# Optimization experiments

Hardware: AMD Instinct MI355X
Metric: run time of the kernel (lower is better)

Reference implementation:

```python
import jax, jax.numpy as jnp
import numpy as np

B, N, C, H = 16, 4096, 256, 4
D = C // H


def setup_inputs() -> dict:
    key = jax.random.key(0)
    ks = jax.random.split(key, 16)
    s = 0.02
    inp = {
        "x": jax.random.normal(ks[0], (B, N, C), jnp.float32),
        "encoding": jax.random.normal(ks[1], (2, B, 1, N, D), jnp.float32),
        "Wqkv_w": jax.random.normal(ks[2], (3 * C, C), jnp.float32) * s,
        "Wqkv_b": jnp.zeros((3 * C,), jnp.float32),
        "tssa_qkv_w": jax.random.normal(ks[3], (C, C), jnp.float32) * s,
        "tssa_qkv_b": jnp.zeros((C,), jnp.float32),
        "temp": jnp.ones((H, 1), jnp.float32),
        "tssa_out_w": jax.random.normal(ks[4], (C, C), jnp.float32) * s,
        "tssa_out_b": jnp.zeros((C,), jnp.float32),
        "out_proj_w": jax.random.normal(ks[5], (C, C), jnp.float32) * s,
        "out_proj_b": jnp.zeros((C,), jnp.float32),
        "ffn1_w": jax.random.normal(ks[6], (2 * C, 2 * C), jnp.float32) * s,
        "ffn1_b": jnp.zeros((2 * C,), jnp.float32),
        "ln_g": jnp.ones((2 * C,), jnp.float32),
        "ln_b": jnp.zeros((2 * C,), jnp.float32),
        "ffn2_w": jax.random.normal(ks[7], (C, 2 * C), jnp.float32) * s,
        "ffn2_b": jnp.zeros((C,), jnp.float32),
    }
    return inp


def _rotate_half(t):
    # (..., d) -> pairwise rotate: (x1, x2) -> (-x2, x1)
    t2 = t.reshape(t.shape[:-1] + (-1, 2))
    x1, x2 = t2[..., 0], t2[..., 1]
    return jnp.stack((-x2, x1), axis=-1).reshape(t.shape)


def reference(x, encoding, Wqkv_w, Wqkv_b, tssa_qkv_w, tssa_qkv_b, temp,
              tssa_out_w, tssa_out_b, out_proj_w, out_proj_b,
              ffn1_w, ffn1_b, ln_g, ln_b, ffn2_w, ffn2_b):
    b, n, c = x.shape
    h, d = H, D
    # QKV projection, layout (h, d, 3) on last dim as in unflatten(-1,(h,-1,3))
    qkv = (x @ Wqkv_w.T + Wqkv_b).reshape(b, n, h, d, 3).transpose(0, 2, 1, 3, 4)  # b h n d 3
    q, k, v = qkv[..., 0], qkv[..., 1], qkv[..., 2]
    rope = lambda t: t * encoding[0] + _rotate_half(t) * encoding[1]
    q = rope(q)
    k = rope(k)
    flat = lambda t: t.transpose(0, 2, 1, 3).reshape(b, n, c)  # b h n d -> b n (h d)
    w_input = (flat(q) + flat(k) + flat(v)) / 3.0
    # TSSA attention
    w = (w_input @ tssa_qkv_w.T + tssa_qkv_b).reshape(b, n, h, d).transpose(0, 2, 1, 3)  # b h n d
    norm = jnp.sqrt(jnp.sum(w * w, axis=2, keepdims=True))  # L2 over sequence axis N
    w_normed = w / jnp.maximum(norm, 1e-12)
    sum_ws = jnp.sum(w_normed * w_normed, axis=-1)  # b h n
    Pi = jax.nn.softmax(sum_ws * temp[None, :, :], axis=1)  # softmax over heads
    Pi_norm = Pi / (jnp.sum(Pi, axis=-1, keepdims=True) + 1e-8)
    dots = jnp.einsum('bhn,bhnd->bh', Pi_norm, w * w)  # (b,h,1,d) summed over d
    attn = 1.0 / (1.0 + dots)  # b h
    out = -(w * Pi[..., None]) * attn[:, :, None, None]  # b h n d
    out = out.transpose(0, 2, 1, 3).reshape(b, n, c)
    context = out @ tssa_out_w.T + tssa_out_b
    message = context @ out_proj_w.T + out_proj_b
    # residual FFN
    cat = jnp.concatenate([x, message], axis=-1)  # b n 2c
    h1 = cat @ ffn1_w.T + ffn1_b
    mu = jnp.mean(h1, axis=-1, keepdims=True)
    var = jnp.mean((h1 - mu) ** 2, axis=-1, keepdims=True)
    ln = (h1 - mu) / jnp.sqrt(var + 1e-5) * ln_g + ln_b
    g = jax.nn.gelu(ln, approximate=False)
    return x + (g @ ffn2_w.T + ffn2_b)
```

## Files before the change

### kernel.cpp

```cpp
#include <hip/hip_runtime.h>
#include <math.h>

#define Bc 16
#define Nc 4096

typedef __attribute__((ext_vector_type(8))) short short8;
typedef __attribute__((ext_vector_type(4))) float floatx4;

__device__ __forceinline__ unsigned short f2bf(float f) {
    union { float f; unsigned int u; } v; v.f = f;
    unsigned int u = v.u;
    return (unsigned short)((u + 0x7fffu + ((u >> 16) & 1u)) >> 16);
}
__device__ __forceinline__ float bf2f(unsigned short u) {
    union { unsigned int u; float f; } v; v.u = ((unsigned int)u) << 16;
    return v.f;
}

__device__ __forceinline__ void gll16(const unsigned short* g, unsigned short* l) {
    __builtin_amdgcn_global_load_lds(
        (const __attribute__((address_space(1))) void*)g,
        (__attribute__((address_space(3))) void*)l,
        16, 0, 0);
}

template <int EPI, typename TOUT>
__global__ __launch_bounds__(512) void gemm_bf(
    const unsigned short* __restrict__ A0, int lda0,
    const unsigned short* __restrict__ A1, int lda1, int K0,
    const unsigned short* __restrict__ W,
    const float* __restrict__ bias,
    const unsigned short* __restrict__ resid_bf,
    const float* __restrict__ Pi,
    const float* __restrict__ attnb,
    float* __restrict__ norm2,
    float* __restrict__ rowstats,
    TOUT* __restrict__ C, int N, int K)
{
    __shared__ alignas(16) unsigned short As[128 * 64];
    __shared__ alignas(16) unsigned short Bs[256 * 64];

    const int t = threadIdx.x;
    const int bn = blockIdx.x, bm = blockIdx.y;
    const int lane = t & 63, wave = t >> 6;
    const int wm = wave >> 2, wn = wave & 3;
    const int quad = lane >> 4, l16 = lane & 15;
    const int rt = t >> 3, st = t & 7;

    floatx4 acc[4][4];
    #pragma unroll
    for (int i = 0; i < 4; ++i)
        #pragma unroll
        for (int j = 0; j < 4; ++j)
            acc[i][j] = (floatx4){0.f, 0.f, 0.f, 0.f};

    for (int k0 = 0; k0 < K; k0 += 64) {
        #pragma unroll
        for (int hh = 0; hh < 2; ++hh) {
            const int row = hh * 64 + rt;
            const int col = k0 + (st ^ (row & 7)) * 8;
            unsigned short* ldsa = As + row * 64 + st * 8;
            const size_t grow = (size_t)bm * 128 + row;
            if constexpr (EPI == 2) {
                const int b = (int)(grow >> 12);
                const int hd = col >> 6;
                const float sc = -Pi[grow * 4 + hd] * attnb[b * 4 + hd];
                const short8 a = *(const short8*)(A0 + grow * (size_t)lda0 + col);
                short8 o;
                #pragma unroll
                for (int j = 0; j < 8; ++j) o[j] = (short)f2bf(bf2f((unsigned short)a[j]) * sc);
                *(short8*)ldsa = o;
            } else {
                const unsigned short* src = (col < K0)
                    ? (A0 + grow * (size_t)lda0 + col)
                    : (A1 + grow * (size_t)lda1 + (col - K0));
                gll16(src, ldsa);
            }
        }
        #pragma unroll
        for (int hh = 0; hh < 4; ++hh) {
            const int row = hh * 64 + rt;
            const int col = k0 + (st ^ (row & 7)) * 8;
            gll16(W + ((size_t)bn * 256 + row) * (size_t)K + col, Bs + row * 64 + st * 8);
        }
        __syncthreads();
        #pragma unroll
        for (int kk = 0; kk < 2; ++kk) {
            short8 af[4], wf[4];
            #pragma unroll
            for (int i = 0; i < 4; ++i) {
                const int ra = wm * 64 + i * 16 + l16;
                af[i] = *(const short8*)(As + ra * 64 + ((quad + kk * 4) ^ (ra & 7)) * 8);
                const int rw = wn * 64 + i * 16 + l16;
                wf[i] = *(const short8*)(Bs + rw * 64 + ((quad + kk * 4) ^ (rw & 7)) * 8);
            }
            #pragma unroll
            for (int mi = 0; mi < 4; ++mi)
                #pragma unroll
                for (int ni = 0; ni < 4; ++ni)
                    acc[mi][ni] = __builtin_amdgcn_mfma_f32_16x16x32_bf16(
                        wf[ni], af[mi], acc[mi][ni], 0, 0, 0);
        }
        __syncthreads();
    }

    float rs[4], rq[4];
    if constexpr (EPI == 4) {
        #pragma unroll
        for (int m = 0; m < 4; ++m) { rs[m] = 0.f; rq[m] = 0.f; }
    }

    #pragma unroll
    for (int mi = 0; mi < 4; ++mi) {
        const size_t row = (size_t)bm * 128 + wm * 64 + mi * 16 + l16;
        #pragma unroll
        for (int ni = 0; ni < 4; ++ni) {
            const int cb = bn * 256 + wn * 64 + ni * 16 + quad * 4;
            const float4 b4 = *(const float4*)(bias + cb);
            float v[4] = {acc[mi][ni][0] + b4.x, acc[mi][ni][1] + b4.y,
                          acc[mi][ni][2] + b4.z, acc[mi][ni][3] + b4.w};
            if constexpr (EPI == 3) {
                const ushort4 xr = *(const ushort4*)(resid_bf + row * (size_t)N + cb);
                v[0] += bf2f(xr.x); v[1] += bf2f(xr.y);
                v[2] += bf2f(xr.z); v[3] += bf2f(xr.w);
            }
            if constexpr (EPI == 4) {
                #pragma unroll
                for (int rg = 0; rg < 4; ++rg) { rs[mi] += v[rg]; rq[mi] += v[rg] * v[rg]; }
            }
            if constexpr (EPI == 1) {
                float cs[4];
                #pragma unroll
                for (int rg = 0; rg < 4; ++rg) cs[rg] = v[rg] * v[rg];
                #pragma unroll
                for (int rg = 0; rg < 4; ++rg) {
                    float s = cs[rg];
                    s += __shfl_xor(s, 1, 64);
                    s += __shfl_xor(s, 2, 64);
                    s += __shfl_xor(s, 4, 64);
                    s += __shfl_xor(s, 8, 64);
                    if (l16 == 0) atomicAdd(&norm2[(bm >> 5) * 256 + cb + rg], s);
                }
            }
            if constexpr (__is_same(TOUT, float)) {
                float4 o; o.x = v[0]; o.y = v[1]; o.z = v[2]; o.w = v[3];
                *(float4*)(C + row * (size_t)N + cb) = o;
            } else {
                ushort4 o;
                o.x = f2bf(v[0]); o.y = f2bf(v[1]); o.z = f2bf(v[2]); o.w = f2bf(v[3]);
                *(ushort4*)(C + row * (size_t)N + cb) = o;
            }
        }
    }
    if constexpr (EPI == 4) {
        #pragma unroll
        for (int mi = 0; mi < 4; ++mi) {
            float s = rs[mi], q = rq[mi];
            s += __shfl_xor(s, 16, 64); s += __shfl_xor(s, 32, 64);
            q += __shfl_xor(q, 16, 64); q += __shfl_xor(q, 32, 64);
            if (quad == 0) {
                const size_t row = (size_t)bm * 128 + wm * 64 + mi * 16 + l16;
                atomicAdd(&rowstats[row * 2], s);
                atomicAdd(&rowstats[row * 2 + 1], q);
            }
        }
    }
}

__global__ __launch_bounds__(256) void gemm_rope(
    const unsigned short* __restrict__ A,
    const unsigned short* __restrict__ Wsv,
    const float* __restrict__ bsv,
    const float* __restrict__ enc,
    unsigned short* __restrict__ wi)
{
    __shared__ alignas(16) unsigned short As[128 * 64];
    __shared__ alignas(16) unsigned short Ss[128 * 64];
    __shared__ alignas(16) unsigned short Vs[128 * 64];

    const int t = threadIdx.x;
    const int bn = blockIdx.x, bm = blockIdx.y;
    const int lane = t & 63, wave = t >> 6;
    const int wm = wave >> 1, wn = wave & 1;
    const int quad = lane >> 4, l16 = lane & 15;
    const int rt = t >> 3, st = t & 7;

    floatx4 accs[4][4], accv[4][4];
    #pragma unroll
    for (int i = 0; i < 4; ++i)
        #pragma unroll
        for (int j = 0; j < 4; ++j) {
            accs[i][j] = (floatx4){0.f, 0.f, 0.f, 0.f};
            accv[i][j] = (floatx4){0.f, 0.f, 0.f, 0.f};
        }

    for (int k0 = 0; k0 < 256; k0 += 64) {
        #pragma unroll
        for (int hh = 0; hh < 4; ++hh) {
            const int row = hh * 32 + rt;
            const int col = k0 + (st ^ (row & 7)) * 8;
            gll16(A + ((size_t)bm * 128 + row) * 256 + col, As + row * 64 + st * 8);
            gll16(Wsv + (size_t)(bn * 128 + row) * 256 + col, Ss + row * 64 + st * 8);
            gll16(Wsv + (size_t)(256 + bn * 128 + row) * 256 + col, Vs + row * 64 + st * 8);
        }
        __syncthreads();
        #pragma unroll
        for (int kk = 0; kk < 2; ++kk) {
            short8 af[4], sf[4], vf[4];
            #pragma unroll
            for (int i = 0; i < 4; ++i) {
                const int ra = wm * 64 + i * 16 + l16;
                af[i] = *(const short8*)(As + ra * 64 + ((quad + kk * 4) ^ (ra & 7)) * 8);
                const int rw = wn * 64 + i * 16 + l16;
                sf[i] = *(const short8*)(Ss + rw * 64 + ((quad + kk * 4) ^ (rw & 7)) * 8);
                vf[i] = *(const short8*)(Vs + rw * 64 + ((quad + kk * 4) ^ (rw & 7)) * 8);
            }
            #pragma unroll
            for (int mi = 0; mi < 4; ++mi)
                #pragma unroll
                for (int ni = 0; ni < 4; ++ni) {
                    accs[mi][ni] = __builtin_amdgcn_mfma_f32_16x16x32_bf16(sf[ni], af[mi], accs[mi][ni], 0, 0, 0);
                    accv[mi][ni] = __builtin_amdgcn_mfma_f32_16x16x32_bf16(vf[ni], af[mi], accv[mi][ni], 0, 0, 0);
                }
        }
        __syncthreads();
    }

    #pragma unroll
    for (int mi = 0; mi < 4; ++mi) {
        const size_t row = (size_t)bm * 128 + wm * 64 + mi * 16 + l16;
        #pragma unroll
        for (int ni = 0; ni < 4; ++ni) {
            const int cb = bn * 128 + wn * 64 + ni * 16 + quad * 4;
            const int d = cb & 63;
            const float s0 = accs[mi][ni][0] + bsv[cb];
            const float s1 = accs[mi][ni][1] + bsv[cb + 1];
            const float s2 = accs[mi][ni][2] + bsv[cb + 2];
            const float s3 = accs[mi][ni][3] + bsv[cb + 3];
            const float v0 = accv[mi][ni][0] + bsv[256 + cb];
            const float v1 = accv[mi][ni][1] + bsv[256 + cb + 1];
            const float v2 = accv[mi][ni][2] + bsv[256 + cb + 2];
            const float v3 = accv[mi][ni][3] + bsv[256 + cb + 3];
            const float4 e0q = *(const float4*)(enc + row * 64 + d);
            const float4 e1q = *(const float4*)(enc + 4194304 + row * 64 + d);
            const float r0 = s0 * e0q.x - s1 * e1q.x;
            const float r1 = s1 * e0q.y + s0 * e1q.y;
            const float r2 = s2 * e0q.z - s3 * e1q.z;
            const float r3 = s3 * e0q.w + s2 * e1q.w;
            ushort4 o;
            o.x = f2bf((r0 + v0) * (1.f / 3.f));
            o.y = f2bf((r1 + v1) * (1.f / 3.f));
            o.z = f2bf((r2 + v2) * (1.f / 3.f));
            o.w = f2bf((r3 + v3) * (1.f / 3.f));
            *(ushort4*)(wi + row * 256 + cb) = o;
        }
    }
}

__global__ __launch_bounds__(256) void lngelu_kernel(unsigned short* __restrict__ h1,
                                                     const float* __restrict__ rowstats,
                                                     const float* __restrict__ g,
                                                     const float* __restrict__ bb) {
    const size_t gid = (size_t)blockIdx.x * 256 + threadIdx.x;
    const size_t row = gid >> 6;
    const int col = (int)(gid & 63) * 8;
    const float2 stv = *(const float2*)(rowstats + row * 2);
    const float mean = stv.x * (1.f / 512.f);
    const float var = stv.y * (1.f / 512.f) - mean * mean;
    const float rstd = rsqrtf(var + 1e-5f);
    unsigned short* p = h1 + row * 512 + col;
    const short8 hv = *(const short8*)p;
    const float4 g0 = *(const float4*)(g + col);
    const float4 g1 = *(const float4*)(g + col + 4);
    const float4 b0 = *(const float4*)(bb + col);
    const float4 b1 = *(const float4*)(bb + col + 4);
    const float vg[8] = {g0.x, g0.y, g0.z, g0.w, g1.x, g1.y, g1.z, g1.w};
    const float vb[8] = {b0.x, b0.y, b0.z, b0.w, b1.x, b1.y, b1.z, b1.w};
    short8 ov;
    #pragma unroll
    for (int k = 0; k < 8; ++k) {
        const float ln = (bf2f((unsigned short)hv[k]) - mean) * rstd * vg[k] + vb[k];
        ov[k] = (short)f2bf(0.5f * ln * (1.f + erff(ln * 0.70710678118654752f)));
    }
    *(short8*)p = ov;
}

__device__ __forceinline__ void conv8(const float* src, unsigned short* dst, int i) {
    const float4 f0 = *(const float4*)(src + (size_t)i * 8);
    const float4 f1 = *(const float4*)(src + (size_t)i * 8 + 4);
    short8 sv;
    sv[0] = (short)f2bf(f0.x); sv[1] = (short)f2bf(f0.y);
    sv[2] = (short)f2bf(f0.z); sv[3] = (short)f2bf(f0.w);
    sv[4] = (short)f2bf(f1.x); sv[5] = (short)f2bf(f1.y);
    sv[6] = (short)f2bf(f1.z); sv[7] = (short)f2bf(f1.w);
    *(short8*)(dst + (size_t)i * 8) = sv;
}

__global__ __launch_bounds__(256) void prep_all(
    const float* __restrict__ x, const float* __restrict__ Wqkv,
    const float* __restrict__ bqkv, const float* __restrict__ tssa_w,
    const float* __restrict__ op_w, const float* __restrict__ to_w,
    const float* __restrict__ to_b, const float* __restrict__ op_b,
    const float* __restrict__ f1w, const float* __restrict__ f2w,
    unsigned short* __restrict__ x_bf, unsigned short* __restrict__ Wsv,
    float* __restrict__ bsv, unsigned short* __restrict__ tssa_bf,
    unsigned short* __restrict__ Wf, float* __restrict__ bfb,
    unsigned short* __restrict__ ffn1_bf, unsigned short* __restrict__ ffn2_bf,
    float* __restrict__ zbase, float* __restrict__ rowstats)
{
    const int blk = blockIdx.x, tt = threadIdx.x;
    if (blk < 8192) {
        conv8(x, x_bf, blk * 256 + tt);
    } else if (blk < 8704) {
        const int r = blk - 8192, c = tt;
        const int cd = r & 255;
        const int h = cd >> 6, dd = cd & 63;
        const int base = h * 192 + dd * 3;
        if (r < 256) {
            Wsv[r * 256 + c] = f2bf(Wqkv[(base + 0) * 256 + c] + Wqkv[(base + 1) * 256 + c]);
            if (c == 0) bsv[r] = bqkv[base] + bqkv[base + 1];
        } else {
            Wsv[r * 256 + c] = f2bf(Wqkv[(base + 2) * 256 + c]);
            if (c == 0) bsv[r] = bqkv[base + 2];
        }
    } else if (blk < 8960) {
        const int i = blk - 8704;
        float s = 0.f;
        for (int k = 0; k < 256; ++k) s += op_w[i * 256 + k] * to_w[k * 256 + tt];
        Wf[i * 256 + tt] = f2bf(s);
    } else if (blk == 8960) {
        float s = op_b[tt];
        for (int k = 0; k < 256; ++k) s += op_w[tt * 256 + k] * to_b[k];
        bfb[tt] = s;
    } else if (blk < 8993) {
        conv8(tssa_w, tssa_bf, (blk - 8961) * 256 + tt);
    } else if (blk < 9121) {
        conv8(f1w, ffn1_bf, (blk - 8993) * 256 + tt);
    } else if (blk < 9185) {
        conv8(f2w, ffn2_bf, (blk - 9121) * 256 + tt);
    } else {
        const int i = (blk - 9185) * 256 + tt;
        if (i < 4288) zbase[i] = 0.f;
        else if (i < 135360) rowstats[i - 4288] = 0.f;
    }
}

__global__ __launch_bounds__(256) void pi_kernel(const unsigned short* __restrict__ w,
                                                 const float* __restrict__ norm2,
                                                 const float* __restrict__ temp,
                                                 float* __restrict__ Pi,
                                                 float* __restrict__ S,
                                                 float* __restrict__ T) {
    const int t = threadIdx.x;
    const int i = t & 15;
    const int lr = t >> 4;
    const size_t r = (size_t)blockIdx.x * 16 + lr;
    const int b = (int)(r >> 12);
    const unsigned short* wrow = w + r * 256;
    const float* n2row = norm2 + b * 256;
    float raw[4], nrm[4];
    #pragma unroll
    for (int h = 0; h < 4; ++h) {
        const ushort4 wv = *(const ushort4*)(wrow + h * 64 + i * 4);
        const float w0 = bf2f(wv.x), w1 = bf2f(wv.y), w2 = bf2f(wv.z), w3 = bf2f(wv.w);
        const float4 n2 = *(const float4*)(n2row + h * 64 + i * 4);
        const float s0 = w0 * w0, s1 = w1 * w1, s2 = w2 * w2, s3 = w3 * w3;
        raw[h] = s0 + s1 + s2 + s3;
        nrm[h] = s0 / fmaxf(n2.x, 1e-24f) + s1 / fmaxf(n2.y, 1e-24f)
               + s2 / fmaxf(n2.z, 1e-24f) + s3 / fmaxf(n2.w, 1e-24f);
    }
    #pragma unroll
    for (int off = 1; off < 16; off <<= 1) {
        #pragma unroll
        for (int h = 0; h < 4; ++h) {
            raw[h] += __shfl_xor(raw[h], off, 64);
            nrm[h] += __shfl_xor(nrm[h], off, 64);
        }
    }
    float sw[4], m = -1e30f;
    #pragma unroll
    for (int h = 0; h < 4; ++h) { sw[h] = nrm[h] * temp[h]; m = fmaxf(m, sw[h]); }
    float e[4], Z = 0.f;
    #pragma unroll
    for (int h = 0; h < 4; ++h) { e[h] = expf(sw[h] - m); Z += e[h]; }
    const float invZ = 1.f / Z;
    float pi[4];
    #pragma unroll
    for (int h = 0; h < 4; ++h) pi[h] = e[h] * invZ;
    if (i < 4) Pi[r * 4 + i] = pi[i];

    __shared__ float sS[16][4], sT[16][4];
    if (i == 0) {
        #pragma unroll
        for (int h = 0; h < 4; ++h) { sS[lr][h] = pi[h]; sT[lr][h] = pi[h] * raw[h]; }
    }
    __syncthreads();
    if (t < 4) {
        float as = 0.f, at = 0.f;
        for (int rr = 0; rr < 16; ++rr) { as += sS[rr][t]; at += sT[rr][t]; }
        atomicAdd(&S[b * 4 + t], as);
        atomicAdd(&T[b * 4 + t], at);
    }
}

__global__ void attn_kernel(const float* __restrict__ S, const float* __restrict__ T,
                            float* __restrict__ attn) {
    const int i = threadIdx.x;
    const float dots = T[i] / (S[i] + 1e-8f);
    attn[i] = 1.f / (1.f + dots);
}

extern "C" void kernel_launch(void* const* d_in, const int* in_sizes, int n_in,
                              void* d_out, int out_size, void* d_ws, size_t ws_size,
                              hipStream_t stream) {
    (void)in_sizes; (void)n_in; (void)out_size; (void)ws_size;
    const float* x          = (const float*)d_in[0];
    const float* enc        = (const float*)d_in[1];
    const float* Wqkv_w     = (const float*)d_in[2];
    const float* Wqkv_b     = (const float*)d_in[3];
    const float* tssa_qkv_w = (const float*)d_in[4];
    const float* tssa_qkv_b = (const float*)d_in[5];
    const float* temp       = (const float*)d_in[6];
    const float* tssa_out_w = (const float*)d_in[7];
    const float* tssa_out_b = (const float*)d_in[8];
    const float* out_proj_w = (const float*)d_in[9];
    const float* out_proj_b = (const float*)d_in[10];
    const float* ffn1_w     = (const float*)d_in[11];
    const float* ffn1_b     = (const float*)d_in[12];
    const float* ln_g       = (const float*)d_in[13];
    const float* ln_b       = (const float*)d_in[14];
    const float* ffn2_w     = (const float*)d_in[15];
    const float* ffn2_b     = (const float*)d_in[16];
    float* outp = (float*)d_out;

    const int M = Bc * Nc;

    char* ws = (char*)d_ws;
    unsigned short* x_bf  = (unsigned short*)(ws);
    unsigned short* wi_bf = (unsigned short*)(ws + (size_t)(32 << 20));
    unsigned short* h1_bf = (unsigned short*)(ws + (size_t)(32 << 20));
    unsigned short* w_bf  = (unsigned short*)(ws + (size_t)(64 << 20));
    unsigned short* msg_bf= (unsigned short*)(ws + (size_t)(96 << 20));
    float* fb    = (float*)(ws + (size_t)(128 << 20));
    float* Pi    = fb;
    float* norm2 = Pi + 262144;
    float* Sb    = norm2 + 4096;
    float* Tb    = Sb + 64;
    float* attnb = Tb + 64;
    float* bsv   = attnb + 64;
    float* bfb   = bsv + 512;
    float* rowstats = bfb + 256;
    unsigned short* Wsv_bf  = (unsigned short*)(rowstats + 131072);
    unsigned short* tssa_bf = Wsv_bf + 131072;
    unsigned short* Wf_bf   = tssa_bf + 65536;
    unsigned short* ffn1_bf = Wf_bf + 65536;
    unsigned short* ffn2_bf = ffn1_bf + 262144;

    prep_all<<<9714, 256, 0, stream>>>(
        x, Wqkv_w, Wqkv_b, tssa_qkv_w, out_proj_w, tssa_out_w, tssa_out_b,
        out_proj_b, ffn1_w, ffn2_w,
        x_bf, Wsv_bf, bsv, tssa_bf, Wf_bf, bfb, ffn1_bf, ffn2_bf,
        norm2, rowstats);

    gemm_rope<<<dim3(2, M / 128), 256, 0, stream>>>(x_bf, Wsv_bf, bsv, enc, wi_bf);

    gemm_bf<1, unsigned short><<<dim3(1, M / 128), 512, 0, stream>>>(
        wi_bf, 256, wi_bf, 256, 256, tssa_bf, tssa_qkv_b,
        nullptr, nullptr, nullptr, norm2, nullptr, w_bf, 256, 256);

    pi_kernel<<<4096, 256, 0, stream>>>(w_bf, norm2, temp, Pi, Sb, Tb);
    attn_kernel<<<1, 64, 0, stream>>>(Sb, Tb, attnb);

    gemm_bf<2, unsigned short><<<dim3(1, M / 128), 512, 0, stream>>>(
        w_bf, 256, w_bf, 256, 256, Wf_bf, bfb,
        nullptr, Pi, attnb, nullptr, nullptr, msg_bf, 256, 256);

    gemm_bf<4, unsigned short><<<dim3(2, M / 128), 512, 0, stream>>>(
        x_bf, 256, msg_bf, 256, 256, ffn1_bf, ffn1_b,
        nullptr, nullptr, nullptr, nullptr, rowstats, h1_bf, 512, 512);

    lngelu_kernel<<<16384, 256, 0, stream>>>(h1_bf, rowstats, ln_g, ln_b);

    gemm_bf<3, float><<<dim3(1, M / 128), 512, 0, stream>>>(
        h1_bf, 512, h1_bf, 512, 512, ffn2_bf, ffn2_b,
        x_bf, nullptr, nullptr, nullptr, nullptr, outp, 256, 512);
}
```

Before: 444.9 us.

## Fuse LayerNorm+GELU into FFN2 A-load and fold RoPE GEMM into generic GEMM

Removes the standalone LayerNorm+GELU kernel and applies the normalisation and erf-GELU while loading A tiles in the FFN2 GEMM, so h1 no longer takes an extra read-modify-write pass through memory. It also replaces the dedicated dual-accumulator RoPE GEMM with the generic 512-thread GEMM template. Wsv rows are interleaved (sum/v alternating) so each 4-wide accumulator holds an s/v pair, and the RoPE epilogue writes half-width outputs. The trade-off is that GELU is recomputed for every N tile, and the A-path in FFN2 now goes through registers instead of async global-to-LDS loads.

New measurement: 471.7 us. 6.0% more time.

```diff
diff --git a/kernel.cpp b/kernel.cpp
--- a/kernel.cpp
+++ b/kernel.cpp
@@ -35,6 +35,9 @@
     const float* __restrict__ attnb,
     float* __restrict__ norm2,
     float* __restrict__ rowstats,
+    const float* __restrict__ enc,
+    const float* __restrict__ lng,
+    const float* __restrict__ lnb,
     TOUT* __restrict__ C, int N, int K)
 {
     __shared__ alignas(16) unsigned short As[128 * 64];
@@ -69,6 +72,24 @@
                 short8 o;
                 #pragma unroll
                 for (int j = 0; j < 8; ++j) o[j] = (short)f2bf(bf2f((unsigned short)a[j]) * sc);
+                *(short8*)ldsa = o;
+            } else if constexpr (EPI == 3) {
+                const float2 stv = *(const float2*)(rowstats + grow * 2);
+                const float mean = stv.x * (1.f / 512.f);
+                const float rstd = rsqrtf(stv.y * (1.f / 512.f) - mean * mean + 1e-5f);
+                const short8 a = *(const short8*)(A0 + grow * (size_t)lda0 + col);
+                const float4 g0 = *(const float4*)(lng + col);
+                const float4 g1 = *(const float4*)(lng + col + 4);
+                const float4 bb0 = *(const float4*)(lnb + col);
+                const float4 bb1 = *(const float4*)(lnb + col + 4);
+                const float vg[8] = {g0.x, g0.y, g0.z, g0.w, g1.x, g1.y, g1.z, g1.w};
+                const float vb[8] = {bb0.x, bb0.y, bb0.z, bb0.w, bb1.x, bb1.y, bb1.z, bb1.w};
+                short8 o;
+                #pragma unroll
+                for (int jj = 0; jj < 8; ++jj) {
+                    const float ln = (bf2f((unsigned short)a[jj]) - mean) * rstd * vg[jj] + vb[jj];
+                    o[jj] = (short)f2bf(0.5f * ln * (1.f + erff(ln * 0.70710678118654752f)));
+                }
                 *(short8*)ldsa = o;
             } else {
                 const unsigned short* src = (col < K0)
@@ -117,38 +138,55 @@
         for (int ni = 0; ni < 4; ++ni) {
             const int cb = bn * 256 + wn * 64 + ni * 16 + quad * 4;
             const float4 b4 = *(const float4*)(bias + cb);
-            float v[4] = {acc[mi][ni][0] + b4.x, acc[mi][ni][1] + b4.y,
-                          acc[mi][ni][2] + b4.z, acc[mi][ni][3] + b4.w};
-            if constexpr (EPI == 3) {
-                const ushort4 xr = *(const ushort4*)(resid_bf + row * (size_t)N + cb);
-                v[0] += bf2f(xr.x); v[1] += bf2f(xr.y);
-                v[2] += bf2f(xr.z); v[3] += bf2f(xr.w);
-            }
-            if constexpr (EPI == 4) {
-                #pragma unroll
-                for (int rg = 0; rg < 4; ++rg) { rs[mi] += v[rg]; rq[mi] += v[rg] * v[rg]; }
-            }
-            if constexpr (EPI == 1) {
-                float cs[4];
-                #pragma unroll
-                for (int rg = 0; rg < 4; ++rg) cs[rg] = v[rg] * v[rg];
-                #pragma unroll
-                for (int rg = 0; rg < 4; ++rg) {
-                    float s = cs[rg];
-                    s += __shfl_xor(s, 1, 64);
-                    s += __shfl_xor(s, 2, 64);
-                    s += __shfl_xor(s, 4, 64);
-                    s += __shfl_xor(s, 8, 64);
-                    if (l16 == 0) atomicAdd(&norm2[(bm >> 5) * 256 + cb + rg], s);
+            if constexpr (EPI == 5) {
+                const float s0 = acc[mi][ni][0] + b4.x;
+                const float v0 = acc[mi][ni][1] + b4.y;
+                const float s1 = acc[mi][ni][2] + b4.z;
+                const float v1 = acc[mi][ni][3] + b4.w;
+                const int j = cb >> 1;
+                const int d = j & 63;
+                const float2 e0 = *(const float2*)(enc + row * 64 + d);
+                const float2 e1 = *(const float2*)(enc + 4194304 + row * 64 + d);
+                const float r0 = s0 * e0.x - s1 * e1.x;
+                const float r1 = s1 * e0.y + s0 * e1.y;
+                ushort2 o;
+                o.x = f2bf((r0 + v0) * (1.f / 3.f));
+                o.y = f2bf((r1 + v1) * (1.f / 3.f));
+                *(ushort2*)((unsigned short*)C + row * (size_t)N + j) = o;
+            } else {
+                float v[4] = {acc[mi][ni][0] + b4.x, acc[mi][ni][1] + b4.y,
+                              acc[mi][ni][2] + b4.z, acc[mi][ni][3] + b4.w};
+                if constexpr (EPI == 3) {
+                    const ushort4 xr = *(const ushort4*)(resid_bf + row * (size_t)N + cb);
+                    v[0] += bf2f(xr.x); v[1] += bf2f(xr.y);
+                    v[2] += bf2f(xr.z); v[3] += bf2f(xr.w);
                 }
-            }
-            if constexpr (__is_same(TOUT, float)) {
-                float4 o; o.x = v[0]; o.y = v[1]; o.z = v[2]; o.w = v[3];
-                *(float4*)(C + row * (size_t)N + cb) = o;
-            } else {
-                ushort4 o;
-                o.x = f2bf(v[0]); o.y = f2bf(v[1]); o.z = f2bf(v[2]); o.w = f2bf(v[3]);
-                *(ushort4*)(C + row * (size_t)N + cb) = o;
+                if constexpr (EPI == 4) {
+                    #pragma unroll
+                    for (int rg = 0; rg < 4; ++rg) { rs[mi] += v[rg]; rq[mi] += v[rg] * v[rg]; }
+                }
+                if constexpr (EPI == 1) {
+                    float cs[4];
+                    #pragma unroll
+                    for (int rg = 0; rg < 4; ++rg) cs[rg] = v[rg] * v[rg];
+                    #pragma unroll
+                    for (int rg = 0; rg < 4; ++rg) {
+                        float s = cs[rg];
+                        s += __shfl_xor(s, 1, 64);
+                        s += __shfl_xor(s, 2, 64);
+                        s += __shfl_xor(s, 4, 64);
+                        s += __shfl_xor(s, 8, 64);
+                        if (l16 == 0) atomicAdd(&norm2[(bm >> 5) * 256 + cb + rg], s);
+                    }
+                }
+                if constexpr (__is_same(TOUT, float)) {
+                    float4 o; o.x = v[0]; o.y = v[1]; o.z = v[2]; o.w = v[3];
+                    *(float4*)(C + row * (size_t)N + cb) = o;
+                } else {
+                    ushort4 o;
+                    o.x = f2bf(v[0]); o.y = f2bf(v[1]); o.z = f2bf(v[2]); o.w = f2bf(v[3]);
+                    *(ushort4*)(C + row * (size_t)N + cb) = o;
+                }
             }
         }
     }
@@ -165,124 +203,6 @@
             }
         }
     }
-}
-
-__global__ __launch_bounds__(256) void gemm_rope(
-    const unsigned short* __restrict__ A,
-    const unsigned short* __restrict__ Wsv,
-    const float* __restrict__ bsv,
-    const float* __restrict__ enc,
-    unsigned short* __restrict__ wi)
-{
-    __shared__ alignas(16) unsigned short As[128 * 64];
-    __shared__ alignas(16) unsigned short Ss[128 * 64];
-    __shared__ alignas(16) unsigned short Vs[128 * 64];
-
-    const int t = threadIdx.x;
-    const int bn = blockIdx.x, bm = blockIdx.y;
-    const int lane = t & 63, wave = t >> 6;
-    const int wm = wave >> 1, wn = wave & 1;
-    const int quad = lane >> 4, l16 = lane & 15;
-    const int rt = t >> 3, st = t & 7;
-
-    floatx4 accs[4][4], accv[4][4];
-    #pragma unroll
-    for (int i = 0; i < 4; ++i)
-        #pragma unroll
-        for (int j = 0; j < 4; ++j) {
-            accs[i][j] = (floatx4){0.f, 0.f, 0.f, 0.f};
-            accv[i][j] = (floatx4){0.f, 0.f, 0.f, 0.f};
-        }
-
-    for (int k0 = 0; k0 < 256; k0 += 64) {
-        #pragma unroll
-        for (int hh = 0; hh < 4; ++hh) {
-            const int row = hh * 32 + rt;
-            const int col = k0 + (st ^ (row & 7)) * 8;
-            gll16(A + ((size_t)bm * 128 + row) * 256 + col, As + row * 64 + st * 8);
-            gll16(Wsv + (size_t)(bn * 128 + row) * 256 + col, Ss + row * 64 + st * 8);
-            gll16(Wsv + (size_t)(256 + bn * 128 + row) * 256 + col, Vs + row * 64 + st * 8);
-        }
-        __syncthreads();
-        #pragma unroll
-        for (int kk = 0; kk < 2; ++kk) {
-            short8 af[4], sf[4], vf[4];
-            #pragma unroll
-            for (int i = 0; i < 4; ++i) {
-                const int ra = wm * 64 + i * 16 + l16;
-                af[i] = *(const short8*)(As + ra * 64 + ((quad + kk * 4) ^ (ra & 7)) * 8);
-                const int rw = wn * 64 + i * 16 + l16;
-                sf[i] = *(const short8*)(Ss + rw * 64 + ((quad + kk * 4) ^ (rw & 7)) * 8);
-                vf[i] = *(const short8*)(Vs + rw * 64 + ((quad + kk * 4) ^ (rw & 7)) * 8);
-            }
-            #pragma unroll
-            for (int mi = 0; mi < 4; ++mi)
-                #pragma unroll
-                for (int ni = 0; ni < 4; ++ni) {
-                    accs[mi][ni] = __builtin_amdgcn_mfma_f32_16x16x32_bf16(sf[ni], af[mi], accs[mi][ni], 0, 0, 0);
-                    accv[mi][ni] = __builtin_amdgcn_mfma_f32_16x16x32_bf16(vf[ni], af[mi], accv[mi][ni], 0, 0, 0);
-                }
-        }
-        __syncthreads();
-    }
-
-    #pragma unroll
-    for (int mi = 0; mi < 4; ++mi) {
-        const size_t row = (size_t)bm * 128 + wm * 64 + mi * 16 + l16;
-        #pragma unroll
-        for (int ni = 0; ni < 4; ++ni) {
-            const int cb = bn * 128 + wn * 64 + ni * 16 + quad * 4;
-            const int d = cb & 63;
-            const float s0 = accs[mi][ni][0] + bsv[cb];
-            const float s1 = accs[mi][ni][1] + bsv[cb + 1];
-            const float s2 = accs[mi][ni][2] + bsv[cb + 2];
-            const float s3 = accs[mi][ni][3] + bsv[cb + 3];
-            const float v0 = accv[mi][ni][0] + bsv[256 + cb];
-            const float v1 = accv[mi][ni][1] + bsv[256 + cb + 1];
-            const float v2 = accv[mi][ni][2] + bsv[256 + cb + 2];
-            const float v3 = accv[mi][ni][3] + bsv[256 + cb + 3];
-            const float4 e0q = *(const float4*)(enc + row * 64 + d);
-            const float4 e1q = *(const float4*)(enc + 4194304 + row * 64 + d);
-            const float r0 = s0 * e0q.x - s1 * e1q.x;
-            const float r1 = s1 * e0q.y + s0 * e1q.y;
-            const float r2 = s2 * e0q.z - s3 * e1q.z;
-            const float r3 = s3 * e0q.w + s2 * e1q.w;
-            ushort4 o;
-            o.x = f2bf((r0 + v0) * (1.f / 3.f));
-            o.y = f2bf((r1 + v1) * (1.f / 3.f));
-            o.z = f2bf((r2 + v2) * (1.f / 3.f));
-            o.w = f2bf((r3 + v3) * (1.f / 3.f));
-            *(ushort4*)(wi + row * 256 + cb) = o;
-        }
-    }
-}
-
-__global__ __launch_bounds__(256) void lngelu_kernel(unsigned short* __restrict__ h1,
-                                                     const float* __restrict__ rowstats,
-                                                     const float* __restrict__ g,
-                                                     const float* __restrict__ bb) {
-    const size_t gid = (size_t)blockIdx.x * 256 + threadIdx.x;
-    const size_t row = gid >> 6;
-    const int col = (int)(gid & 63) * 8;
-    const float2 stv = *(const float2*)(rowstats + row * 2);
-    const float mean = stv.x * (1.f / 512.f);
-    const float var = stv.y * (1.f / 512.f) - mean * mean;
-    const float rstd = rsqrtf(var + 1e-5f);
-    unsigned short* p = h1 + row * 512 + col;
-    const short8 hv = *(const short8*)p;
-    const float4 g0 = *(const float4*)(g + col);
-    const float4 g1 = *(const float4*)(g + col + 4);
-    const float4 b0 = *(const float4*)(bb + col);
-    const float4 b1 = *(const float4*)(bb + col + 4);
-    const float vg[8] = {g0.x, g0.y, g0.z, g0.w, g1.x, g1.y, g1.z, g1.w};
-    const float vb[8] = {b0.x, b0.y, b0.z, b0.w, b1.x, b1.y, b1.z, b1.w};
-    short8 ov;
-    #pragma unroll
-    for (int k = 0; k < 8; ++k) {
-        const float ln = (bf2f((unsigned short)hv[k]) - mean) * rstd * vg[k] + vb[k];
-        ov[k] = (short)f2bf(0.5f * ln * (1.f + erff(ln * 0.70710678118654752f)));
-    }
-    *(short8*)p = ov;
 }
 
 __device__ __forceinline__ void conv8(const float* src, unsigned short* dst, int i) {
@@ -313,10 +233,10 @@
         conv8(x, x_bf, blk * 256 + tt);
     } else if (blk < 8704) {
         const int r = blk - 8192, c = tt;
-        const int cd = r & 255;
-        const int h = cd >> 6, dd = cd & 63;
+        const int j = r >> 1;
+        const int h = j >> 6, dd = j & 63;
         const int base = h * 192 + dd * 3;
-        if (r < 256) {
+        if (!(r & 1)) {
             Wsv[r * 256 + c] = f2bf(Wqkv[(base + 0) * 256 + c] + Wqkv[(base + 1) * 256 + c]);
             if (c == 0) bsv[r] = bqkv[base] + bqkv[base + 1];
         } else {
@@ -462,26 +382,31 @@
         x_bf, Wsv_bf, bsv, tssa_bf, Wf_bf, bfb, ffn1_bf, ffn2_bf,
         norm2, rowstats);
 
-    gemm_rope<<<dim3(2, M / 128), 256, 0, stream>>>(x_bf, Wsv_bf, bsv, enc, wi_bf);
+    gemm_bf<5, unsigned short><<<dim3(2, M / 128), 512, 0, stream>>>(
+        x_bf, 256, x_bf, 256, 256, Wsv_bf, bsv,
+        nullptr, nullptr, nullptr, nullptr, nullptr,
+        enc, nullptr, nullptr, wi_bf, 256, 256);
 
     gemm_bf<1, unsigned short><<<dim3(1, M / 128), 512, 0, stream>>>(
         wi_bf, 256, wi_bf, 256, 256, tssa_bf, tssa_qkv_b,
-        nullptr, nullptr, nullptr, norm2, nullptr, w_bf, 256, 256);
+        nullptr, nullptr, nullptr, norm2, nullptr,
+        nullptr, nullptr, nullptr, w_bf, 256, 256);
 
     pi_kernel<<<4096, 256, 0, stream>>>(w_bf, norm2, temp, Pi, Sb, Tb);
     attn_kernel<<<1, 64, 0, stream>>>(Sb, Tb, attnb);
 
     gemm_bf<2, unsigned short><<<dim3(1, M / 128), 512, 0, stream>>>(
         w_bf, 256, w_bf, 256, 256, Wf_bf, bfb,
-        nullptr, Pi, attnb, nullptr, nullptr, msg_bf, 256, 256);
+        nullptr, Pi, attnb, nullptr, nullptr,
+        nullptr, nullptr, nullptr, msg_bf, 256, 256);
 
     gemm_bf<4, unsigned short><<<dim3(2, M / 128), 512, 0, stream>>>(
         x_bf, 256, msg_bf, 256, 256, ffn1_bf, ffn1_b,
-        nullptr, nullptr, nullptr, nullptr, rowstats, h1_bf, 512, 512);
-
-    lngelu_kernel<<<16384, 256, 0, stream>>>(h1_bf, rowstats, ln_g, ln_b);
+        nullptr, nullptr, nullptr, nullptr, rowstats,
+        nullptr, nullptr, nullptr, h1_bf, 512, 512);
 
     gemm_bf<3, float><<<dim3(1, M / 128), 512, 0, stream>>>(
         h1_bf, 512, h1_bf, 512, 512, ffn2_bf, ffn2_b,
-        x_bf, nullptr, nullptr, nullptr, nullptr, outp, 256, 512);
-}
+        x_bf, nullptr, nullptr, nullptr, rowstats,
+        nullptr, ln_g, ln_b, outp, 256, 512);
+}
```

## Fuse LayerNorm+GELU into FFN2 A-load and attn scalar into message GEMM

Applied to the files above, without the earlier changes.

Removes the standalone LayerNorm/GELU kernel by applying normalization and GELU while staging h1 tiles into shared memory inside the FFN2 GEMM. The attention scalar is now computed from S and T inside the message GEMM instead of a separate tiny kernel. GELU now uses a polynomial erf approximation with __expf. This cuts one full read and write pass over h1 and two launches. In exchange, the FFN2 A path moves from async global_load_lds to register loads plus per-element math, which could slow the GEMM's main loop.

Measured after the change: 466.9 us. +4.9%, slower.

```diff
diff --git a/kernel.cpp b/kernel.cpp
--- a/kernel.cpp
+++ b/kernel.cpp
@@ -15,6 +15,17 @@
 __device__ __forceinline__ float bf2f(unsigned short u) {
     union { unsigned int u; float f; } v; v.u = ((unsigned int)u) << 16;
     return v.f;
+}
+
+__device__ __forceinline__ float gelu_f(float x) {
+    const float z = x * 0.70710678118654752f;
+    const float az = fabsf(z);
+    const float t = 1.f / (1.f + 0.3275911f * az);
+    const float poly = t * (0.254829592f + t * (-0.284496736f +
+                       t * (1.421413741f + t * (-1.453152027f + t * 1.061405429f))));
+    const float e = __expf(-z * z);
+    const float er = copysignf(1.f - poly * e, z);
+    return 0.5f * x * (1.f + er);
 }
 
 __device__ __forceinline__ void gll16(const unsigned short* g, unsigned short* l) {
@@ -32,9 +43,12 @@
     const float* __restrict__ bias,
     const unsigned short* __restrict__ resid_bf,
     const float* __restrict__ Pi,
-    const float* __restrict__ attnb,
+    const float* __restrict__ Sb,
+    const float* __restrict__ Tb,
     float* __restrict__ norm2,
     float* __restrict__ rowstats,
+    const float* __restrict__ lng,
+    const float* __restrict__ lnb,
     TOUT* __restrict__ C, int N, int K)
 {
     __shared__ alignas(16) unsigned short As[128 * 64];
@@ -46,6 +60,17 @@
     const int wm = wave >> 2, wn = wave & 3;
     const int quad = lane >> 4, l16 = lane & 15;
     const int rt = t >> 3, st = t & 7;
+
+    float mean0 = 0.f, rstd0 = 0.f, mean1 = 0.f, rstd1 = 0.f;
+    if constexpr (EPI == 3) {
+        const size_t g0 = (size_t)bm * 128 + rt;
+        const float2 s0 = *(const float2*)(rowstats + g0 * 2);
+        const float2 s1 = *(const float2*)(rowstats + (g0 + 64) * 2);
+        mean0 = s0.x * (1.f / 512.f);
+        rstd0 = rsqrtf(s0.y * (1.f / 512.f) - mean0 * mean0 + 1e-5f);
+        mean1 = s1.x * (1.f / 512.f);
+        rstd1 = rsqrtf(s1.y * (1.f / 512.f) - mean1 * mean1 + 1e-5f);
+    }
 
     floatx4 acc[4][4];
     #pragma unroll
@@ -64,11 +89,30 @@
             if constexpr (EPI == 2) {
                 const int b = (int)(grow >> 12);
                 const int hd = col >> 6;
-                const float sc = -Pi[grow * 4 + hd] * attnb[b * 4 + hd];
+                const float Sv = Sb[b * 4 + hd], Tv = Tb[b * 4 + hd];
+                const float at = 1.f / (1.f + Tv / (Sv + 1e-8f));
+                const float sc = -Pi[grow * 4 + hd] * at;
                 const short8 a = *(const short8*)(A0 + grow * (size_t)lda0 + col);
                 short8 o;
                 #pragma unroll
                 for (int j = 0; j < 8; ++j) o[j] = (short)f2bf(bf2f((unsigned short)a[j]) * sc);
+                *(short8*)ldsa = o;
+            } else if constexpr (EPI == 3) {
+                const float mean = hh ? mean1 : mean0;
+                const float rstd = hh ? rstd1 : rstd0;
+                const short8 a = *(const short8*)(A0 + grow * (size_t)lda0 + col);
+                const float4 ga = *(const float4*)(lng + col);
+                const float4 gb = *(const float4*)(lng + col + 4);
+                const float4 ba = *(const float4*)(lnb + col);
+                const float4 bb = *(const float4*)(lnb + col + 4);
+                const float vg[8] = {ga.x, ga.y, ga.z, ga.w, gb.x, gb.y, gb.z, gb.w};
+                const float vb[8] = {ba.x, ba.y, ba.z, ba.w, bb.x, bb.y, bb.z, bb.w};
+                short8 o;
+                #pragma unroll
+                for (int jj = 0; jj < 8; ++jj) {
+                    const float ln = (bf2f((unsigned short)a[jj]) - mean) * rstd * vg[jj] + vb[jj];
+                    o[jj] = (short)f2bf(gelu_f(ln));
+                }
                 *(short8*)ldsa = o;
             } else {
                 const unsigned short* src = (col < K0)
@@ -255,34 +299,6 @@
             *(ushort4*)(wi + row * 256 + cb) = o;
         }
     }
-}
-
-__global__ __launch_bounds__(256) void lngelu_kernel(unsigned short* __restrict__ h1,
-                                                     const float* __restrict__ rowstats,
-                                                     const float* __restrict__ g,
-                                                     const float* __restrict__ bb) {
-    const size_t gid = (size_t)blockIdx.x * 256 + threadIdx.x;
-    const size_t row = gid >> 6;
-    const int col = (int)(gid & 63) * 8;
-    const float2 stv = *(const float2*)(rowstats + row * 2);
-    const float mean = stv.x * (1.f / 512.f);
-    const float var = stv.y * (1.f / 512.f) - mean * mean;
-    const float rstd = rsqrtf(var + 1e-5f);
-    unsigned short* p = h1 + row * 512 + col;
-    const short8 hv = *(const short8*)p;
-    const float4 g0 = *(const float4*)(g + col);
-    const float4 g1 = *(const float4*)(g + col + 4);
-    const float4 b0 = *(const float4*)(bb + col);
-    const float4 b1 = *(const float4*)(bb + col + 4);
-    const float vg[8] = {g0.x, g0.y, g0.z, g0.w, g1.x, g1.y, g1.z, g1.w};
-    const float vb[8] = {b0.x, b0.y, b0.z, b0.w, b1.x, b1.y, b1.z, b1.w};
-    short8 ov;
-    #pragma unroll
-    for (int k = 0; k < 8; ++k) {
-        const float ln = (bf2f((unsigned short)hv[k]) - mean) * rstd * vg[k] + vb[k];
-        ov[k] = (short)f2bf(0.5f * ln * (1.f + erff(ln * 0.70710678118654752f)));
-    }
-    *(short8*)p = ov;
 }
 
 __device__ __forceinline__ void conv8(const float* src, unsigned short* dst, int i) {
@@ -403,13 +419,6 @@
     }
 }
 
-__global__ void attn_kernel(const float* __restrict__ S, const float* __restrict__ T,
-                            float* __restrict__ attn) {
-    const int i = threadIdx.x;
-    const float dots = T[i] / (S[i] + 1e-8f);
-    attn[i] = 1.f / (1.f + dots);
-}
-
 extern "C" void kernel_launch(void* const* d_in, const int* in_sizes, int n_in,
                               void* d_out, int out_size, void* d_ws, size_t ws_size,
                               hipStream_t stream) {
@@ -466,22 +475,23 @@
 
     gemm_bf<1, unsigned short><<<dim3(1, M / 128), 512, 0, stream>>>(
         wi_bf, 256, wi_bf, 256, 256, tssa_bf, tssa_qkv_b,
-        nullptr, nullptr, nullptr, norm2, nullptr, w_bf, 256, 256);
+        nullptr, nullptr, nullptr, nullptr, norm2, nullptr,
+        nullptr, nullptr, w_bf, 256, 256);
 
     pi_kernel<<<4096, 256, 0, stream>>>(w_bf, norm2, temp, Pi, Sb, Tb);
-    attn_kernel<<<1, 64, 0, stream>>>(Sb, Tb, attnb);
 
     gemm_bf<2, unsigned short><<<dim3(1, M / 128), 512, 0, stream>>>(
         w_bf, 256, w_bf, 256, 256, Wf_bf, bfb,
-        nullptr, Pi, attnb, nullptr, nullptr, msg_bf, 256, 256);
+        nullptr, Pi, Sb, Tb, nullptr, nullptr,
+        nullptr, nullptr, msg_bf, 256, 256);
 
     gemm_bf<4, unsigned short><<<dim3(2, M / 128), 512, 0, stream>>>(
         x_bf, 256, msg_bf, 256, 256, ffn1_bf, ffn1_b,
-        nullptr, nullptr, nullptr, nullptr, rowstats, h1_bf, 512, 512);
-
-    lngelu_kernel<<<16384, 256, 0, stream>>>(h1_bf, rowstats, ln_g, ln_b);
+        nullptr, nullptr, nullptr, nullptr, nullptr, rowstats,
+        nullptr, nullptr, h1_bf, 512, 512);
 
     gemm_bf<3, float><<<dim3(1, M / 128), 512, 0, stream>>>(
         h1_bf, 512, h1_bf, 512, 512, ffn2_bf, ffn2_b,
-        x_bf, nullptr, nullptr, nullptr, nullptr, outp, 256, 512);
-}
+        x_bf, nullptr, nullptr, nullptr, nullptr, rowstats,
+        ln_g, ln_b, outp, 256, 512);
+}
```
